# Performance work log

Hardware: AMD Instinct MI355X
Metric: run time of the kernel (lower is better)

Reference implementation:

```python
import jax, jax.numpy as jnp
import numpy as np

EPS = 1e-16


def setup_inputs() -> dict:
    key = jax.random.key(0)
    k1, k2 = jax.random.split(key)
    p = jax.random.normal(k1, (2, 32, 2048, 4), dtype=jnp.float32)
    q = jax.random.normal(k2, (32, 2048, 4), dtype=jnp.float32)
    return {"p": p, "q": q}


def reference(p, q):
    # im=False path: take the real part of the complex generated momenta
    p_real = p[0]                      # (B, N, 4)
    # loss_norm_choice='p3', take_sqrt=True: use 3-momenta (drop energy)
    p3 = p_real[..., 1:]               # (B, N, 3)
    q3 = q[..., 1:]                    # (B, M, 3)
    # Pairwise Euclidean distance (cdist) via the expanded quadratic form to
    # avoid materializing the (B, N, M, 3) difference tensor.
    x2 = jnp.sum(p3 * p3, axis=-1)     # (B, N)
    y2 = jnp.sum(q3 * q3, axis=-1)     # (B, M)
    xy = jnp.einsum('bnd,bmd->bnm', p3, q3)  # (B, N, M)
    dist_sq = x2[..., :, None] + y2[..., None, :] - 2.0 * xy
    dist = jnp.sqrt(jnp.maximum(dist_sq, 0.0) + EPS)  # (B, N, M)
    # Bidirectional nearest-neighbor min-reduction
    min_pq = jnp.min(dist, axis=-1)    # (B, N)
    min_qp = jnp.min(dist, axis=-2)    # (B, M)
    chamfer_loss = jnp.sum((min_pq + min_qp) * 0.5)
    return chamfer_loss
```

## Files before the change

### kernel.cpp

```cpp
#include <hip/hip_runtime.h>
#include <math.h>


#define NPTS   2048
#define NBATCH 32
#define NBI    16
#define NJH    2
#define WS_ROW_FLOATS ((size_t)NBATCH * NBI * NJH * 128)
#define EPSF   1e-16f
#define BIGF   3.4e38f
#define ONEBF  0x3F80u

typedef __attribute__((ext_vector_type(8)))  short bf16x8;
typedef __attribute__((ext_vector_type(16))) float f32x16;
typedef __attribute__((ext_vector_type(4)))  unsigned int u32x4;

__device__ __forceinline__ float min3f(float a, float b, float c) {
    return fminf(fminf(a, b), c);
}
__device__ __forceinline__ unsigned short bf16_rne(float f) {
    unsigned int u = __float_as_uint(f);
    return (unsigned short)((u + 0x7FFFu + ((u >> 16) & 1u)) >> 16);
}
__device__ __forceinline__ float bf16_f32(unsigned short h) {
    return __uint_as_float(((unsigned int)h) << 16);
}

__global__ __launch_bounds__(256, 4) void chamfer_mfma_kernel(
    const float* __restrict__ P, const float* __restrict__ Q,
    float* __restrict__ ws, float* __restrict__ out)
{
    __shared__ u32x4        sfrag[2][1024];
    __shared__ unsigned int scol[1024];
    __shared__ float        srow[128];

    const int tid  = threadIdx.x;
    const int lane = tid & 63;
    const int wv   = tid >> 6;
    const int l31  = lane & 31;
    const int hi   = lane >> 5;
    const int bi   = blockIdx.x;
    const int jh   = blockIdx.y;
    const int b    = blockIdx.z;

    if (bi == 0 && jh == 0 && b == 0 && tid == 0) *out = 0.f;

    {
        const float4* Qb = (const float4*)Q + (size_t)b * NPTS + jh * 1024;
        #pragma unroll
        for (int s = 0; s < 4; ++s) {
            int c = tid + 256 * s;
            float4 qv = Qb[c];
            float gx = -2.f * qv.y, gy = -2.f * qv.z, gz = -2.f * qv.w;
            unsigned short hx = bf16_rne(gx), hy = bf16_rne(gy), hz = bf16_rne(gz);
            unsigned short lx = bf16_rne(gx - bf16_f32(hx));
            unsigned short ly = bf16_rne(gy - bf16_f32(hy));
            unsigned short lz = bf16_rne(gz - bf16_f32(hz));
            float y2 = fmaf(qv.y, qv.y, fmaf(qv.z, qv.z, qv.w * qv.w));
            unsigned short y2h = bf16_rne(y2);
            unsigned short y2l = bf16_rne(y2 - bf16_f32(y2h));
            sfrag[0][c] = (u32x4){ (unsigned)hx | ((unsigned)hy << 16),
                                   (unsigned)hz | ((unsigned)hx << 16),
                                   (unsigned)hy | ((unsigned)hz << 16),
                                   (unsigned)lx | ((unsigned)ly << 16) };
            sfrag[1][c] = (u32x4){ (unsigned)lz | (ONEBF << 16),
                                   ONEBF | ((unsigned)y2h << 16),
                                   (unsigned)y2l,
                                   0u };
            scol[c] = 0x7F7F7F7Fu;
        }
    }

    bf16x8 afrag;
    {
        const int rowl = wv * 32 + l31;
        float4 pv = ((const float4*)P)[(size_t)b * NPTS + bi * 128 + rowl];
        float x = pv.y, y = pv.z, z = pv.w;
        unsigned short hx = bf16_rne(x), hy = bf16_rne(y), hz = bf16_rne(z);
        unsigned short lx = bf16_rne(x - bf16_f32(hx));
        unsigned short ly = bf16_rne(y - bf16_f32(hy));
        unsigned short lz = bf16_rne(z - bf16_f32(hz));
        float x2 = fmaf(x, x, fmaf(y, y, z * z));
        unsigned short x2h = bf16_rne(x2);
        unsigned short x2l = bf16_rne(x2 - bf16_f32(x2h));
        u32x4 araw;
        if (hi == 0)
            araw = (u32x4){ (unsigned)hx | ((unsigned)hy << 16),
                            (unsigned)hz | ((unsigned)lx << 16),
                            (unsigned)ly | ((unsigned)lz << 16),
                            (unsigned)hx | ((unsigned)hy << 16) };
        else
            araw = (u32x4){ (unsigned)hz | ((unsigned)x2h << 16),
                            (unsigned)x2l | (ONEBF << 16),
                            ONEBF,
                            0u };
        afrag = __builtin_bit_cast(bf16x8, araw);
    }
    __syncthreads();

    const u32x4* bbase = &sfrag[hi][0];
    f32x16 cz;
    #pragma unroll
    for (int r = 0; r < 16; ++r) cz[r] = 0.f;

    float rowacc[16];
    #pragma unroll
    for (int r = 0; r < 16; ++r) rowacc[r] = BIGF;

    for (int t = 0; t < 32; ++t) {
        const int c = t * 32 + l31;
        bf16x8 bfrag = __builtin_bit_cast(bf16x8, bbase[c]);

        f32x16 d = __builtin_amdgcn_mfma_f32_32x32x16_bf16(afrag, bfrag, cz,
                                                           0, 0, 0);
        #pragma unroll
        for (int r = 0; r < 16; ++r) rowacc[r] = fminf(rowacc[r], d[r]);

        float m = fminf(min3f(min3f(d[0], d[1], d[2]),
                              min3f(d[3], d[4], d[5]),
                              min3f(d[6], d[7], d[8])),
                        min3f(min3f(d[9], d[10], d[11]),
                              min3f(d[12], d[13], d[14]), d[15]));
        m = fminf(m, __shfl_xor(m, 32));
        if (hi == 0)
            atomicMin(&scol[c], __float_as_uint(fmaxf(m, 0.f)));
    }

    #pragma unroll
    for (int r = 0; r < 16; ++r) {
        float v = rowacc[r];
        v = fminf(v, __shfl_xor(v, 1));
        v = fminf(v, __shfl_xor(v, 2));
        v = fminf(v, __shfl_xor(v, 4));
        v = fminf(v, __shfl_xor(v, 8));
        v = fminf(v, __shfl_xor(v, 16));
        rowacc[r] = v;
    }
    if (l31 == 0) {
        #pragma unroll
        for (int r = 0; r < 16; ++r)
            srow[wv * 32 + 4 * hi + (r & 3) + 8 * (r >> 2)] = rowacc[r];
    }
    __syncthreads();

    if (tid < 128)
        ws[(((size_t)b * NBI + bi) * NJH + jh) * 128 + tid] = srow[tid];
    {
        float* cbase = ws + WS_ROW_FLOATS
                     + (((size_t)b * NJH + jh) * NBI + bi) * 1024;
        #pragma unroll
        for (int s = 0; s < 4; ++s) {
            int c = tid + 256 * s;
            cbase[c] = __uint_as_float(scol[c]);
        }
    }
}

__global__ __launch_bounds__(256) void chamfer_sum_kernel(
    const float* __restrict__ ws, float* __restrict__ out)
{
    __shared__ float rbuf[4];
    const int tid = threadIdx.x;
    const int i   = blockIdx.x * 256 + tid;
    const int b   = i >> 11;
    const int e   = i & 2047;

    float s;
    {
        const int bi = e >> 7, el = e & 127;
        const float* rb = ws + ((size_t)(b * NBI + bi) * NJH) * 128 + el;
        float v = fminf(rb[0], rb[128]);
        s = sqrtf(fmaxf(v, 0.f) + EPSF);
    }
    {
        const int jh = e >> 10, el = e & 1023;
        const float* cb = ws + WS_ROW_FLOATS
                        + ((size_t)(b * NJH + jh) * NBI) * 1024 + el;
        float v = BIGF;
        #pragma unroll
        for (int j = 0; j < NBI; ++j) v = fminf(v, cb[(size_t)j * 1024]);
        s += sqrtf(fmaxf(v, 0.f) + EPSF);
    }

    #pragma unroll
    for (int off = 32; off > 0; off >>= 1) s += __shfl_down(s, off);
    if ((tid & 63) == 0) rbuf[tid >> 6] = s;
    __syncthreads();
    if (tid == 0)
        atomicAdd(out, 0.5f * ((rbuf[0] + rbuf[1]) + (rbuf[2] + rbuf[3])));
}

extern "C" void kernel_launch(void* const* d_in, const int* in_sizes, int n_in,
                              void* d_out, int out_size, void* d_ws, size_t ws_size,
                              hipStream_t stream) {
    const float* P = (const float*)d_in[0];
    const float* Q = (const float*)d_in[1];
    float* out = (float*)d_out;
    float* ws  = (float*)d_ws;

    dim3 grid(NBI, NJH, NBATCH);
    chamfer_mfma_kernel<<<grid, 256, 0, stream>>>(P, Q, ws, out);
    chamfer_sum_kernel<<<256, 256, 0, stream>>>(ws, out);
}
```

Measured before the change: 84.50 us.

## Switch to 16x16x32 bf16 MFMA with two A fragments and smaller column tiles

Replaces the 32x32x16 MFMA with the 16x16x32 variant. The split-bf16 distance terms are repacked across three B fragment arrays and four lane groups, and each wave issues two MFMAs per B fragment. Column tiles shrink from 1024 to 512, which doubles the grid and halves LDS per block. The aim is to cut the per-tile min-reduction work (4 outputs per lane instead of 16) and raise occupancy and parallelism, at the cost of more atomicMin traffic and more partial results for the sum kernel to reduce.

New measurement: 80.28 us. 1.05x faster.

```diff
diff --git a/kernel.cpp b/kernel.cpp
--- a/kernel.cpp
+++ b/kernel.cpp
@@ -4,16 +4,18 @@
 
 #define NPTS   2048
 #define NBATCH 32
-#define NBI    16
-#define NJH    2
-#define WS_ROW_FLOATS ((size_t)NBATCH * NBI * NJH * 128)
+#define BROWS  128
+#define BCOLS  512
+#define NBI    (NPTS / BROWS)
+#define NJC    (NPTS / BCOLS)
+#define WS_ROW_FLOATS ((size_t)NBATCH * NBI * NJC * BROWS)
 #define EPSF   1e-16f
 #define BIGF   3.4e38f
 #define ONEBF  0x3F80u
 
-typedef __attribute__((ext_vector_type(8)))  short bf16x8;
-typedef __attribute__((ext_vector_type(16))) float f32x16;
-typedef __attribute__((ext_vector_type(4)))  unsigned int u32x4;
+typedef __attribute__((ext_vector_type(8))) short bf16x8;
+typedef __attribute__((ext_vector_type(4))) float f32x4;
+typedef __attribute__((ext_vector_type(4))) unsigned int u32x4;
 
 __device__ __forceinline__ float min3f(float a, float b, float c) {
     return fminf(fminf(a, b), c);
@@ -30,25 +32,27 @@
     const float* __restrict__ P, const float* __restrict__ Q,
     float* __restrict__ ws, float* __restrict__ out)
 {
-    __shared__ u32x4        sfrag[2][1024];
-    __shared__ unsigned int scol[1024];
-    __shared__ float        srow[128];
+    __shared__ u32x4        sB0[BCOLS];
+    __shared__ u32x4        sB1[BCOLS];
+    __shared__ u32x4        sB2[BCOLS];
+    __shared__ unsigned int scol[BCOLS];
+    __shared__ float        srow[BROWS];
 
     const int tid  = threadIdx.x;
     const int lane = tid & 63;
     const int wv   = tid >> 6;
-    const int l31  = lane & 31;
-    const int hi   = lane >> 5;
+    const int c15  = lane & 15;
+    const int g    = lane >> 4;
     const int bi   = blockIdx.x;
-    const int jh   = blockIdx.y;
+    const int jc   = blockIdx.y;
     const int b    = blockIdx.z;
 
-    if (bi == 0 && jh == 0 && b == 0 && tid == 0) *out = 0.f;
-
-    {
-        const float4* Qb = (const float4*)Q + (size_t)b * NPTS + jh * 1024;
-        #pragma unroll
-        for (int s = 0; s < 4; ++s) {
+    if (bi == 0 && jc == 0 && b == 0 && tid == 0) *out = 0.f;
+
+    {
+        const float4* Qb = (const float4*)Q + (size_t)b * NPTS + jc * BCOLS;
+        #pragma unroll
+        for (int s = 0; s < 2; ++s) {
             int c = tid + 256 * s;
             float4 qv = Qb[c];
             float gx = -2.f * qv.y, gy = -2.f * qv.z, gz = -2.f * qv.w;
@@ -59,99 +63,103 @@
             float y2 = fmaf(qv.y, qv.y, fmaf(qv.z, qv.z, qv.w * qv.w));
             unsigned short y2h = bf16_rne(y2);
             unsigned short y2l = bf16_rne(y2 - bf16_f32(y2h));
-            sfrag[0][c] = (u32x4){ (unsigned)hx | ((unsigned)hy << 16),
-                                   (unsigned)hz | ((unsigned)hx << 16),
-                                   (unsigned)hy | ((unsigned)hz << 16),
-                                   (unsigned)lx | ((unsigned)ly << 16) };
-            sfrag[1][c] = (u32x4){ (unsigned)lz | (ONEBF << 16),
-                                   ONEBF | ((unsigned)y2h << 16),
-                                   (unsigned)y2l,
-                                   0u };
+            sB0[c] = (u32x4){ (unsigned)hx | ((unsigned)hy << 16),
+                              (unsigned)hz | ((unsigned)lx << 16),
+                              (unsigned)ly | ((unsigned)lz << 16),
+                              ONEBF | (ONEBF << 16) };
+            sB1[c] = (u32x4){ (unsigned)lx | ((unsigned)ly << 16),
+                              (unsigned)lz | ((unsigned)y2h << 16),
+                              (unsigned)y2l, 0u };
+            sB2[c] = (u32x4){ (unsigned)hx | ((unsigned)hy << 16),
+                              (unsigned)hz, 0u, 0u };
             scol[c] = 0x7F7F7F7Fu;
         }
     }
 
-    bf16x8 afrag;
-    {
-        const int rowl = wv * 32 + l31;
-        float4 pv = ((const float4*)P)[(size_t)b * NPTS + bi * 128 + rowl];
-        float x = pv.y, y = pv.z, z = pv.w;
-        unsigned short hx = bf16_rne(x), hy = bf16_rne(y), hz = bf16_rne(z);
-        unsigned short lx = bf16_rne(x - bf16_f32(hx));
-        unsigned short ly = bf16_rne(y - bf16_f32(hy));
-        unsigned short lz = bf16_rne(z - bf16_f32(hz));
-        float x2 = fmaf(x, x, fmaf(y, y, z * z));
-        unsigned short x2h = bf16_rne(x2);
-        unsigned short x2l = bf16_rne(x2 - bf16_f32(x2h));
-        u32x4 araw;
-        if (hi == 0)
-            araw = (u32x4){ (unsigned)hx | ((unsigned)hy << 16),
-                            (unsigned)hz | ((unsigned)lx << 16),
-                            (unsigned)ly | ((unsigned)lz << 16),
-                            (unsigned)hx | ((unsigned)hy << 16) };
-        else
-            araw = (u32x4){ (unsigned)hz | ((unsigned)x2h << 16),
-                            (unsigned)x2l | (ONEBF << 16),
-                            ONEBF,
-                            0u };
-        afrag = __builtin_bit_cast(bf16x8, araw);
+    bf16x8 afrag0, afrag1;
+    {
+        const float4* Pb = (const float4*)P + (size_t)b * NPTS
+                         + bi * BROWS + wv * 32;
+        #pragma unroll
+        for (int h = 0; h < 2; ++h) {
+            float4 pv = Pb[h * 16 + c15];
+            float x = pv.y, y = pv.z, z = pv.w;
+            unsigned short hx = bf16_rne(x), hy = bf16_rne(y), hz = bf16_rne(z);
+            unsigned short lx = bf16_rne(x - bf16_f32(hx));
+            unsigned short ly = bf16_rne(y - bf16_f32(hy));
+            unsigned short lz = bf16_rne(z - bf16_f32(hz));
+            float x2 = fmaf(x, x, fmaf(y, y, z * z));
+            unsigned short x2h = bf16_rne(x2);
+            unsigned short x2l = bf16_rne(x2 - bf16_f32(x2h));
+            u32x4 a;
+            if (g == 0)
+                a = (u32x4){ (unsigned)hx | ((unsigned)hy << 16),
+                             (unsigned)hz | ((unsigned)lx << 16),
+                             (unsigned)ly | ((unsigned)lz << 16),
+                             (unsigned)x2h | ((unsigned)x2l << 16) };
+            else if (g == 1)
+                a = (u32x4){ (unsigned)hx | ((unsigned)hy << 16),
+                             (unsigned)hz | (ONEBF << 16),
+                             ONEBF, 0u };
+            else if (g == 2)
+                a = (u32x4){ (unsigned)lx | ((unsigned)ly << 16),
+                             (unsigned)lz, 0u, 0u };
+            else
+                a = (u32x4){ 0u, 0u, 0u, 0u };
+            if (h == 0) afrag0 = __builtin_bit_cast(bf16x8, a);
+            else        afrag1 = __builtin_bit_cast(bf16x8, a);
+        }
     }
     __syncthreads();
 
-    const u32x4* bbase = &sfrag[hi][0];
-    f32x16 cz;
+    const u32x4* bbase = (g == 0) ? sB0 : (g == 1) ? sB1 : sB2;
+    const f32x4 cz = {0.f, 0.f, 0.f, 0.f};
+    float ra0[4], ra1[4];
     #pragma unroll
-    for (int r = 0; r < 16; ++r) cz[r] = 0.f;
-
-    float rowacc[16];
+    for (int r = 0; r < 4; ++r) { ra0[r] = BIGF; ra1[r] = BIGF; }
+
+    #pragma unroll 2
+    for (int t = 0; t < BCOLS / 16; ++t) {
+        bf16x8 bfrag = __builtin_bit_cast(bf16x8, bbase[t * 16 + c15]);
+        f32x4 d0 = __builtin_amdgcn_mfma_f32_16x16x32_bf16(afrag0, bfrag, cz, 0, 0, 0);
+        f32x4 d1 = __builtin_amdgcn_mfma_f32_16x16x32_bf16(afrag1, bfrag, cz, 0, 0, 0);
+        #pragma unroll
+        for (int r = 0; r < 4; ++r) {
+            ra0[r] = fminf(ra0[r], d0[r]);
+            ra1[r] = fminf(ra1[r], d1[r]);
+        }
+        float m = min3f(min3f(d0[0], d0[1], d0[2]),
+                        min3f(d0[3], d1[0], d1[1]),
+                        fminf(d1[2], d1[3]));
+        m = fminf(m, __shfl_xor(m, 16));
+        m = fminf(m, __shfl_xor(m, 32));
+        if (lane < 16)
+            atomicMin(&scol[t * 16 + lane], __float_as_uint(fmaxf(m, 0.f)));
+    }
+
     #pragma unroll
-    for (int r = 0; r < 16; ++r) rowacc[r] = BIGF;
-
-    for (int t = 0; t < 32; ++t) {
-        const int c = t * 32 + l31;
-        bf16x8 bfrag = __builtin_bit_cast(bf16x8, bbase[c]);
-
-        f32x16 d = __builtin_amdgcn_mfma_f32_32x32x16_bf16(afrag, bfrag, cz,
-                                                           0, 0, 0);
-        #pragma unroll
-        for (int r = 0; r < 16; ++r) rowacc[r] = fminf(rowacc[r], d[r]);
-
-        float m = fminf(min3f(min3f(d[0], d[1], d[2]),
-                              min3f(d[3], d[4], d[5]),
-                              min3f(d[6], d[7], d[8])),
-                        min3f(min3f(d[9], d[10], d[11]),
-                              min3f(d[12], d[13], d[14]), d[15]));
-        m = fminf(m, __shfl_xor(m, 32));
-        if (hi == 0)
-            atomicMin(&scol[c], __float_as_uint(fmaxf(m, 0.f)));
-    }
-
-    #pragma unroll
-    for (int r = 0; r < 16; ++r) {
-        float v = rowacc[r];
-        v = fminf(v, __shfl_xor(v, 1));
-        v = fminf(v, __shfl_xor(v, 2));
-        v = fminf(v, __shfl_xor(v, 4));
-        v = fminf(v, __shfl_xor(v, 8));
-        v = fminf(v, __shfl_xor(v, 16));
-        rowacc[r] = v;
-    }
-    if (l31 == 0) {
-        #pragma unroll
-        for (int r = 0; r < 16; ++r)
-            srow[wv * 32 + 4 * hi + (r & 3) + 8 * (r >> 2)] = rowacc[r];
+    for (int r = 0; r < 4; ++r) {
+        float v0 = ra0[r], v1 = ra1[r];
+        v0 = fminf(v0, __shfl_xor(v0, 1)); v1 = fminf(v1, __shfl_xor(v1, 1));
+        v0 = fminf(v0, __shfl_xor(v0, 2)); v1 = fminf(v1, __shfl_xor(v1, 2));
+        v0 = fminf(v0, __shfl_xor(v0, 4)); v1 = fminf(v1, __shfl_xor(v1, 4));
+        v0 = fminf(v0, __shfl_xor(v0, 8)); v1 = fminf(v1, __shfl_xor(v1, 8));
+        if (c15 == 0) {
+            srow[wv * 32 + g * 4 + r]      = v0;
+            srow[wv * 32 + 16 + g * 4 + r] = v1;
+        }
     }
     __syncthreads();
 
-    if (tid < 128)
-        ws[(((size_t)b * NBI + bi) * NJH + jh) * 128 + tid] = srow[tid];
-    {
-        float* cbase = ws + WS_ROW_FLOATS
-                     + (((size_t)b * NJH + jh) * NBI + bi) * 1024;
-        #pragma unroll
-        for (int s = 0; s < 4; ++s) {
+    if (tid < BROWS)
+        ws[(((size_t)b * NBI + bi) * NJC + jc) * BROWS + tid] = srow[tid];
+    {
+        float* cb = ws + WS_ROW_FLOATS
+                  + (((size_t)b * NJC + jc) * NBI + bi) * BCOLS;
+        #pragma unroll
+        for (int s = 0; s < 2; ++s) {
             int c = tid + 256 * s;
-            cbase[c] = __uint_as_float(scol[c]);
+            cb[c] = __uint_as_float(scol[c]);
         }
     }
 }
@@ -167,18 +175,19 @@
 
     float s;
     {
-        const int bi = e >> 7, el = e & 127;
-        const float* rb = ws + ((size_t)(b * NBI + bi) * NJH) * 128 + el;
-        float v = fminf(rb[0], rb[128]);
+        const int bi = e >> 7, rl = e & 127;
+        const float* rb = ws + ((size_t)(b * NBI + bi) * NJC) * BROWS + rl;
+        float v = fminf(fminf(rb[0], rb[BROWS]),
+                        fminf(rb[2 * BROWS], rb[3 * BROWS]));
         s = sqrtf(fmaxf(v, 0.f) + EPSF);
     }
     {
-        const int jh = e >> 10, el = e & 1023;
+        const int jcx = e >> 9, cl = e & 511;
         const float* cb = ws + WS_ROW_FLOATS
-                        + ((size_t)(b * NJH + jh) * NBI) * 1024 + el;
+                        + ((size_t)(b * NJC + jcx) * NBI) * BCOLS + cl;
         float v = BIGF;
         #pragma unroll
-        for (int j = 0; j < NBI; ++j) v = fminf(v, cb[(size_t)j * 1024]);
+        for (int j = 0; j < NBI; ++j) v = fminf(v, cb[(size_t)j * BCOLS]);
         s += sqrtf(fmaxf(v, 0.f) + EPSF);
     }
 
@@ -198,7 +207,7 @@
     float* out = (float*)d_out;
     float* ws  = (float*)d_ws;
 
-    dim3 grid(NBI, NJH, NBATCH);
+    dim3 grid(NBI, NJC, NBATCH);
     chamfer_mfma_kernel<<<grid, 256, 0, stream>>>(P, Q, ws, out);
     chamfer_sum_kernel<<<256, 256, 0, stream>>>(ws, out);
 }
```
